# Kernel optimization log

Measured on AMD Instinct MI355X. Metric: run time of the kernel, lower is better.

## Reference

```python
import jax, jax.numpy as jnp
import numpy as np

NUM_NODES = 512
HEADS = 4
IN_F = 256
OUT_F = 128
EPS = 1e-5


def _layernorm(x, g, b):
    mu = jnp.mean(x, axis=-1, keepdims=True)
    var = jnp.mean(jnp.square(x - mu), axis=-1, keepdims=True)
    return (x - mu) * jax.lax.rsqrt(var + EPS) * g + b


def setup_inputs() -> dict:
    key = jax.random.key(0)
    ks = jax.random.split(key, 16)
    N = 32 * NUM_NODES
    E = 262144
    s = 0.05
    return {
        "x": jax.random.normal(ks[0], (N, IN_F), jnp.float32),
        "edge_index": jax.random.randint(ks[1], (2, E), 0, N, jnp.int64),
        "W_l": jax.random.normal(ks[2], (IN_F, HEADS * OUT_F), jnp.float32) * s,
        "W_r": jax.random.normal(ks[3], (IN_F, HEADS * OUT_F), jnp.float32) * s,
        "att": jax.random.normal(ks[4], (HEADS, OUT_F), jnp.float32) * s,
        "gat_bias": jnp.zeros((OUT_F,), jnp.float32),
        "gat_gamma": jnp.ones((OUT_F,), jnp.float32),
        "gat_beta": jnp.zeros((OUT_F,), jnp.float32),
        "cnn_W": jax.random.normal(ks[5], (IN_F, OUT_F), jnp.float32) * s,
        "cnn_b": jnp.zeros((OUT_F,), jnp.float32),
        "conv_W": jax.random.normal(ks[6], (OUT_F, OUT_F, 7), jnp.float32) * s,
        "conv_b": jnp.zeros((OUT_F,), jnp.float32),
        "cnn_gamma": jnp.ones((OUT_F,), jnp.float32),
        "cnn_beta": jnp.zeros((OUT_F,), jnp.float32),
        "res_W": jax.random.normal(ks[7], (IN_F, OUT_F), jnp.float32) * s,
        "res_b": jnp.zeros((OUT_F,), jnp.float32),
        "fuse_gamma": jnp.ones((OUT_F,), jnp.float32),
        "fuse_beta": jnp.zeros((OUT_F,), jnp.float32),
    }


def reference(x, edge_index, W_l, W_r, att, gat_bias, gat_gamma, gat_beta,
              cnn_W, cnn_b, conv_W, conv_b, cnn_gamma, cnn_beta,
              res_W, res_b, fuse_gamma, fuse_beta):
    N = x.shape[0]
    B = N // NUM_NODES
    # --- GATv2 branch (add self-loops like PyG default) ---
    loop = jnp.arange(N, dtype=edge_index.dtype)
    src = jnp.concatenate([edge_index[0], loop])
    dst = jnp.concatenate([edge_index[1], loop])
    x_l = (x @ W_l).reshape(N, HEADS, OUT_F)
    x_r = (x @ W_r).reshape(N, HEADS, OUT_F)
    e = x_l[src] + x_r[dst]                      # [E+N, H, F]
    e = jnp.where(e > 0, e, 0.2 * e)             # leaky_relu, slope 0.2
    score = jnp.einsum('ehf,hf->eh', e, att)     # [E+N, H]
    m = jax.ops.segment_max(score, dst, num_segments=N)
    ex = jnp.exp(score - m[dst])
    denom = jax.ops.segment_sum(ex, dst, num_segments=N)
    alpha = ex / denom[dst]
    agg = jax.ops.segment_sum(alpha[:, :, None] * x_l[src], dst, num_segments=N)
    h_gat = jnp.mean(agg, axis=1) + gat_bias     # concat=False -> head mean
    h_gat = jnp.where(h_gat > 0, h_gat, 0.01 * h_gat)  # nn.LeakyReLU default
    h_gat = _layernorm(h_gat, gat_gamma, gat_beta)
    # --- CNN branch ---
    xc = x @ cnn_W + cnn_b                       # [N, F]
    xc = xc.reshape(B, NUM_NODES, OUT_F).transpose(0, 2, 1)  # [B, F, L]
    hc = jax.lax.conv_general_dilated(xc, conv_W, window_strides=(1,),
                                      padding=[(3, 3)],
                                      dimension_numbers=('NCW', 'OIW', 'NCW'))
    hc = hc + conv_b[None, :, None]
    hc = hc.transpose(0, 2, 1).reshape(N, OUT_F)
    hc = jax.nn.relu(hc)
    hc = _layernorm(hc, cnn_gamma, cnn_beta)
    # --- fuse + residual ---
    h = h_gat + hc + (x @ res_W + res_b)
    return _layernorm(h, fuse_gamma, fuse_beta)
```

## Files before the change

### kernel.cpp

```cpp
#include <hip/hip_runtime.h>
#include <hip/hip_bf16.h>
#include <math.h>

#define IN_F 256
#define OUT_F 128
#define HEADS 4
#define HF 512
#define NCAT 1280

typedef __hip_bfloat16 bf16;
typedef unsigned short ushort_t;
typedef unsigned char uchar_t;

using bf16x8 = __attribute__((ext_vector_type(8))) short;
using f32x4  = __attribute__((ext_vector_type(4))) float;

__device__ __forceinline__ float bflo(unsigned u) { return __uint_as_float(u << 16); }
__device__ __forceinline__ float bfhi(unsigned u) { return __uint_as_float(u & 0xffff0000u); }
__device__ __forceinline__ float bf2f(ushort_t u) { return __uint_as_float((unsigned)u << 16); }
__device__ __forceinline__ ushort_t f2bf(float f) {
    __hip_bfloat16 h = __float2bfloat16(f);
    return *reinterpret_cast<ushort_t*>(&h);
}

__device__ __forceinline__ void gload16(const void* g, void* l) {
    __builtin_amdgcn_global_load_lds(
        (const __attribute__((address_space(1))) unsigned int*)g,
        (__attribute__((address_space(3))) unsigned int*)l, 16, 0, 0);
}

template <int CTRL>
__device__ __forceinline__ float dpp_add(float s) {
    int t = __builtin_amdgcn_update_dpp(0, __float_as_int(s), CTRL, 0xf, 0xf, true);
    return s + __int_as_float(t);
}
__device__ __forceinline__ float rowsum16(float s) {
    s = dpp_add<0x121>(s);
    s = dpp_add<0x122>(s);
    s = dpp_add<0x124>(s);
    s = dpp_add<0x128>(s);
    return s;
}

__global__ __launch_bounds__(256) void prep_kernel(
    const float* __restrict__ x, ushort_t* __restrict__ xb, int n_cvt,
    const float* __restrict__ Wl, const float* __restrict__ Wr,
    const float* __restrict__ Wc, const float* __restrict__ Wres,
    const float* __restrict__ Wconv,
    ushort_t* __restrict__ Wt, ushort_t* __restrict__ Wt2,
    const int* __restrict__ ei, int* __restrict__ counts, int E,
    int g1, int g2) {
    int b = blockIdx.x;
    if (b < g1) {
        int i = (b * 256 + threadIdx.x) * 8;
        if (i >= n_cvt) return;
        float4 a = *(const float4*)(x + i);
        float4 c = *(const float4*)(x + i + 4);
        uint4 o;
        o.x = f2bf(a.x) | ((unsigned)f2bf(a.y) << 16);
        o.y = f2bf(a.z) | ((unsigned)f2bf(a.w) << 16);
        o.z = f2bf(c.x) | ((unsigned)f2bf(c.y) << 16);
        o.w = f2bf(c.z) | ((unsigned)f2bf(c.w) << 16);
        *(uint4*)(xb + i) = o;
    } else if (b < g2) {
        int idx = (b - g1) * 256 + threadIdx.x;
        if (idx < NCAT * 256) {
            int n = idx >> 8, k = idx & 255;
            float v;
            if (n < 512)       v = Wl[(size_t)k * 512 + n];
            else if (n < 1024) v = Wr[(size_t)k * 512 + (n - 512)];
            else if (n < 1152) v = Wc[(size_t)k * 128 + (n - 1024)];
            else               v = Wres[(size_t)k * 128 + (n - 1152)];
            Wt[idx] = f2bf(v);
        } else {
            int j = idx - NCAT * 256;
            if (j < 7 * 128 * 128) {
                int k = j >> 14, o = (j >> 7) & 127, i = j & 127;
                Wt2[j] = f2bf(Wconv[((size_t)o * 128 + i) * 7 + k]);
            }
        }
    } else {
        int e = (b - g2) * 256 + threadIdx.x;
        if (e < E) atomicAdd(&counts[ei[E + e]], 1);
    }
}

__global__ __launch_bounds__(256) void gemm_scatter_kernel(
    const ushort_t* __restrict__ A,
    const ushort_t* __restrict__ Wt,
    uchar_t* __restrict__ xl8t, float* __restrict__ scales,
    ushort_t* __restrict__ xrb, ushort_t* __restrict__ xcb,
    ushort_t* __restrict__ resb,
    const int* __restrict__ ei, int* __restrict__ cursor,
    int* __restrict__ srcs, int E, int SB) {
    __shared__ __align__(1024) ushort_t As[128 * 64];
    __shared__ __align__(1024) ushort_t Bs[128 * 64];
    __shared__ float smax[128][2];
    if (blockIdx.x < SB) {
        int e = blockIdx.x * 256 + threadIdx.x;
        if (e < E) {
            int dd = ei[E + e];
            int pp = atomicAdd(&cursor[dd], 1);
            srcs[pp] = ei[e];
        }
        return;
    }
    int bid = blockIdx.x - SB;
    int by = bid / 10, bx = bid - by * 10;
    int tid = threadIdx.x;
    int lane = tid & 63, wid = tid >> 6;
    int wr = (wid >> 1) * 64, wc = (wid & 1) * 64;
    int brow = by * 128, bcol = bx * 128;
    int srow = lane >> 3;
    int sslot = lane & 7;
    int rl = lane & 15, kq = lane >> 4;
    f32x4 acc[4][4] = {};
    for (int k0 = 0; k0 < 256; k0 += 64) {
        #pragma unroll
        for (int j = 0; j < 4; ++j) {
            int r = (wid * 4 + j) * 8 + srow;
            int sl = sslot ^ (r & 7);
            gload16(A  + (size_t)(brow + r) * 256 + k0 + sl * 8,
                    (char*)As + (wid * 4 + j) * 1024);
            gload16(Wt + (size_t)(bcol + r) * 256 + k0 + sl * 8,
                    (char*)Bs + (wid * 4 + j) * 1024);
        }
        __syncthreads();
        #pragma unroll
        for (int ks = 0; ks < 2; ++ks) {
            int cb = ks * 64 + kq * 16;
            bf16x8 af[4], bfv[4];
            #pragma unroll
            for (int m = 0; m < 4; ++m) {
                int r = wr + m * 16 + rl;
                af[m] = *(const bf16x8*)((const char*)As + r * 128 + (cb ^ ((r & 7) << 4)));
            }
            #pragma unroll
            for (int n = 0; n < 4; ++n) {
                int r = wc + n * 16 + rl;
                bfv[n] = *(const bf16x8*)((const char*)Bs + r * 128 + (cb ^ ((r & 7) << 4)));
            }
            #pragma unroll
            for (int m = 0; m < 4; ++m)
                #pragma unroll
                for (int n = 0; n < 4; ++n)
                    acc[m][n] = __builtin_amdgcn_mfma_f32_16x16x32_bf16(
                        af[m], bfv[n], acc[m][n], 0, 0, 0);
        }
        __syncthreads();
    }
    int rowb = kq * 4;
    if (bcol < 512) {
        int head = bcol >> 7;
        float rmax[4][4];
        #pragma unroll
        for (int m = 0; m < 4; ++m)
            #pragma unroll
            for (int q = 0; q < 4; ++q) {
                float t = fabsf(acc[m][0][q]);
                t = fmaxf(t, fabsf(acc[m][1][q]));
                t = fmaxf(t, fabsf(acc[m][2][q]));
                t = fmaxf(t, fabsf(acc[m][3][q]));
                #pragma unroll
                for (int o = 1; o < 16; o <<= 1) t = fmaxf(t, __shfl_xor(t, o));
                rmax[m][q] = t;
            }
        if (rl == 0) {
            #pragma unroll
            for (int m = 0; m < 4; ++m)
                #pragma unroll
                for (int q = 0; q < 4; ++q)
                    smax[wr + m * 16 + rowb + q][wid & 1] = rmax[m][q];
        }
        __syncthreads();
        #pragma unroll
        for (int m = 0; m < 4; ++m)
            #pragma unroll
            for (int q = 0; q < 4; ++q) {
                int row = wr + m * 16 + rowb + q;
                float sm = fmaxf(fmaxf(smax[row][0], smax[row][1]), 1e-8f);
                float s = sm * (1.f / 127.f);
                float rs = 127.f / sm;
                if ((wid & 1) == 0 && rl == 0)
                    scales[(size_t)(brow + row) * 4 + head] = s;
                #pragma unroll
                for (int n = 0; n < 4; ++n) {
                    int col = bcol + wc + n * 16 + rl;
                    int qv = (int)rintf(acc[m][n][q] * rs) + 128;
                    xl8t[(size_t)(brow + row) * 512 + col] = (uchar_t)qv;
                }
            }
        return;
    }
    ushort_t* dstp; int cstride, cb2;
    if (bcol < 1024)      { dstp = xrb;  cstride = 512; cb2 = bcol - 512; }
    else if (bcol < 1152) { dstp = xcb;  cstride = 128; cb2 = bcol - 1024; }
    else                  { dstp = resb; cstride = 128; cb2 = bcol - 1152; }
    #pragma unroll
    for (int m = 0; m < 4; ++m)
        #pragma unroll
        for (int n = 0; n < 4; ++n) {
            int col = cb2 + wc + n * 16 + rl;
            #pragma unroll
            for (int q = 0; q < 4; ++q) {
                int row = brow + wr + m * 16 + rowb + q;
                dstp[(size_t)row * cstride + col] = f2bf(acc[m][n][q]);
            }
        }
}

__global__ __launch_bounds__(1024) void scan_kernel(
    const int* __restrict__ counts, int* __restrict__ offs,
    int* __restrict__ cursor, int N) {
    __shared__ int wsum[16];
    int t = threadIdx.x;
    int lane = t & 63, w = t >> 6;
    int base = t * 16;
    int local[16], s = 0;
    #pragma unroll
    for (int i = 0; i < 16; ++i) {
        int v = (base + i < N) ? counts[base + i] : 0;
        local[i] = v; s += v;
    }
    int sc = s;
    #pragma unroll
    for (int off = 1; off < 64; off <<= 1) {
        int v = __shfl_up(sc, off);
        if (lane >= off) sc += v;
    }
    if (lane == 63) wsum[w] = sc;
    __syncthreads();
    if (w == 0 && lane < 16) {
        int v = wsum[lane];
        int scv = v;
        #pragma unroll
        for (int off = 1; off < 16; off <<= 1) {
            int u = __shfl_up(scv, off);
            if (lane >= off) scv += u;
        }
        wsum[lane] = scv - v;
    }
    __syncthreads();
    int run = wsum[w] + sc - s;
    #pragma unroll
    for (int i = 0; i < 16; ++i) {
        if (base + i < N) { offs[base + i] = run; cursor[base + i] = run; }
        run += local[i];
    }
}

__global__ __launch_bounds__(256) void conv_ln_kernel(
    const ushort_t* __restrict__ xcb, const float* __restrict__ cnn_b,
    const ushort_t* __restrict__ Wt2, const float* __restrict__ conv_b,
    const float* __restrict__ cnn_gamma, const float* __restrict__ cnn_beta,
    ushort_t* __restrict__ hcn_ln) {
    __shared__ ushort_t As[38][136];
    __shared__ __align__(1024) ushort_t Bs[128 * 128];
    __shared__ float hbuf[32][129];
    int tid = threadIdx.x;
    int lane = tid & 63, wid = tid >> 6;
    int wr = (wid >> 1) * 16, wc = (wid & 1) * 64;
    int b = blockIdx.y, l0 = blockIdx.x * 32;
    for (int u = tid; u < 38 * 16; u += 256) {
        int r = u >> 4, seg = u & 15;
        int l = l0 - 3 + r;
        uint4 o4 = make_uint4(0, 0, 0, 0);
        if (l >= 0 && l < 512) {
            uint4 v = *(const uint4*)(xcb + (size_t)(b * 512 + l) * 128 + seg * 8);
            float4 b0 = *(const float4*)(cnn_b + seg * 8);
            float4 b1 = *(const float4*)(cnn_b + seg * 8 + 4);
            o4.x = f2bf(bflo(v.x) + b0.x) | ((unsigned)f2bf(bfhi(v.x) + b0.y) << 16);
            o4.y = f2bf(bflo(v.y) + b0.z) | ((unsigned)f2bf(bfhi(v.y) + b0.w) << 16);
            o4.z = f2bf(bflo(v.z) + b1.x) | ((unsigned)f2bf(bfhi(v.z) + b1.y) << 16);
            o4.w = f2bf(bflo(v.w) + b1.z) | ((unsigned)f2bf(bfhi(v.w) + b1.w) << 16);
        }
        *(uint4*)&As[r][seg * 8] = o4;
    }
    f32x4 acc[4] = {};
    int rl = lane & 15, kb = (lane >> 4) * 8;
    int sr4 = lane >> 4, ss = lane & 15;
    for (int k = 0; k < 7; ++k) {
        __syncthreads();
        #pragma unroll
        for (int j = 0; j < 8; ++j) {
            int r = (wid * 8 + j) * 4 + sr4;
            int sl = ss ^ (r & 15);
            gload16(Wt2 + ((size_t)(k * 128 + r)) * 128 + sl * 8,
                    (char*)Bs + (wid * 8 + j) * 1024);
        }
        __syncthreads();
        #pragma unroll
        for (int kk = 0; kk < 4; ++kk) {
            bf16x8 af = *(const bf16x8*)&As[wr + rl + k][kk * 32 + kb];
            int cbyte = kk * 64 + (lane >> 4) * 16;
            #pragma unroll
            for (int n = 0; n < 4; ++n) {
                int r = wc + n * 16 + rl;
                bf16x8 bfr = *(const bf16x8*)((const char*)Bs + r * 256
                                              + (cbyte ^ ((r & 15) << 4)));
                acc[n] = __builtin_amdgcn_mfma_f32_16x16x32_bf16(af, bfr, acc[n], 0, 0, 0);
            }
        }
    }
    __syncthreads();
    int rowb = (lane >> 4) * 4;
    #pragma unroll
    for (int n = 0; n < 4; ++n) {
        int col = wc + n * 16 + rl;
        float cb = conv_b[col];
        #pragma unroll
        for (int q = 0; q < 4; ++q) {
            int r = wr + rowb + q;
            hbuf[r][col] = fmaxf(acc[n][q] + cb, 0.f);
        }
    }
    __syncthreads();
    for (int r = wid * 8; r < wid * 8 + 8; ++r) {
        int grow = b * 512 + l0 + r;
        float h0 = hbuf[r][lane], h1 = hbuf[r][lane + 64];
        float s = h0 + h1;
        #pragma unroll
        for (int off = 32; off; off >>= 1) s += __shfl_xor(s, off);
        float mu = s * (1.f / 128.f);
        float d0 = h0 - mu, d1 = h1 - mu;
        float vs = d0 * d0 + d1 * d1;
        #pragma unroll
        for (int off = 32; off; off >>= 1) vs += __shfl_xor(vs, off);
        float inv = rsqrtf(vs * (1.f / 128.f) + 1e-5f);
        size_t base = (size_t)grow * 128;
        hcn_ln[base + lane]      = f2bf(d0 * inv * cnn_gamma[lane]      + cnn_beta[lane]);
        hcn_ln[base + lane + 64] = f2bf(d1 * inv * cnn_gamma[lane + 64] + cnn_beta[lane + 64]);
    }
}

__global__ __launch_bounds__(256) void gat_final_kernel(
    const uchar_t* __restrict__ xl8t, const float* __restrict__ scales,
    const ushort_t* __restrict__ xrb,
    const int* __restrict__ srcs, const int* __restrict__ offs,
    const float* __restrict__ att, const float* __restrict__ gat_bias,
    const float* __restrict__ gat_gamma, const float* __restrict__ gat_beta,
    const ushort_t* __restrict__ hcn_ln, const ushort_t* __restrict__ resb,
    const float* __restrict__ res_b,
    const float* __restrict__ fuse_gamma, const float* __restrict__ fuse_beta,
    float* __restrict__ out, int E, int N) {
    int wid = (blockIdx.x * 256 + threadIdx.x) >> 6;
    int lane = threadIdx.x & 63;
    if (wid >= N) return;
    int d = wid;
    int h = lane >> 4;
    const uint4 rv = ((const uint4*)(xrb + (size_t)d * HF))[lane];
    float xr8[8];
    xr8[0] = bflo(rv.x); xr8[1] = bfhi(rv.x);
    xr8[2] = bflo(rv.y); xr8[3] = bfhi(rv.y);
    xr8[4] = bflo(rv.z); xr8[5] = bfhi(rv.z);
    xr8[6] = bflo(rv.w); xr8[7] = bfhi(rv.w);
    const float LOG2E = 1.44269504f;
    const float4 a0 = ((const float4*)att)[lane * 2];
    const float4 a1 = ((const float4*)att)[lane * 2 + 1];
    const float aw[8] = {a0.x * LOG2E, a0.y * LOG2E, a0.z * LOG2E, a0.w * LOG2E,
                         a1.x * LOG2E, a1.y * LOG2E, a1.z * LOG2E, a1.w * LOG2E};
    float acc[8] = {};
    float dn = 0.f, sumexs = 0.f;

    auto process = [&](uint2 lv, float sc) {
        float qf[8];
        qf[0] = (float)(lv.x & 0xff);         qf[1] = (float)((lv.x >> 8) & 0xff);
        qf[2] = (float)((lv.x >> 16) & 0xff); qf[3] = (float)(lv.x >> 24);
        qf[4] = (float)(lv.y & 0xff);         qf[5] = (float)((lv.y >> 8) & 0xff);
        qf[6] = (float)((lv.y >> 16) & 0xff); qf[7] = (float)(lv.y >> 24);
        float c = 128.f * sc;
        float s1 = 0.f, s2 = 0.f;
        #pragma unroll
        for (int j = 0; j < 8; ++j) {
            float v = fmaf(sc, qf[j], xr8[j]) - c;
            s1 = fmaf(v, aw[j], s1);
            s2 = fmaf(fabsf(v), aw[j], s2);
        }
        float s = fmaf(0.6f, s1, 0.4f * s2);
        s = rowsum16(s);
        float ex = exp2f(s);
        float exs = ex * sc;
        dn += ex; sumexs += exs;
        #pragma unroll
        for (int j = 0; j < 8; ++j) acc[j] = fmaf(exs, qf[j], acc[j]);
    };

    process(((const uint2*)(xl8t + (size_t)d * 512))[lane],
            scales[(size_t)d * 4 + h]);

    int start = offs[d];
    int end = (d == N - 1) ? E : offs[d + 1];
    int nfull = (end - start) >> 2;
    int p = start;
    uint2 L0, L1, L2, L3;
    float C0, C1, C2, C3;
    if (nfull > 0) {
        int s0 = srcs[p], s1 = srcs[p + 1], s2 = srcs[p + 2], s3 = srcs[p + 3];
        L0 = ((const uint2*)(xl8t + (size_t)s0 * 512))[lane];
        L1 = ((const uint2*)(xl8t + (size_t)s1 * 512))[lane];
        L2 = ((const uint2*)(xl8t + (size_t)s2 * 512))[lane];
        L3 = ((const uint2*)(xl8t + (size_t)s3 * 512))[lane];
        C0 = scales[(size_t)s0 * 4 + h];
        C1 = scales[(size_t)s1 * 4 + h];
        C2 = scales[(size_t)s2 * 4 + h];
        C3 = scales[(size_t)s3 * 4 + h];
        p += 4;
    }
    for (int b = 1; b < nfull; ++b) {
        int s0 = srcs[p], s1 = srcs[p + 1], s2 = srcs[p + 2], s3 = srcs[p + 3];
        uint2 M0 = ((const uint2*)(xl8t + (size_t)s0 * 512))[lane];
        uint2 M1 = ((const uint2*)(xl8t + (size_t)s1 * 512))[lane];
        uint2 M2 = ((const uint2*)(xl8t + (size_t)s2 * 512))[lane];
        uint2 M3 = ((const uint2*)(xl8t + (size_t)s3 * 512))[lane];
        float D0 = scales[(size_t)s0 * 4 + h];
        float D1 = scales[(size_t)s1 * 4 + h];
        float D2 = scales[(size_t)s2 * 4 + h];
        float D3 = scales[(size_t)s3 * 4 + h];
        p += 4;
        process(L0, C0); process(L1, C1); process(L2, C2); process(L3, C3);
        L0 = M0; L1 = M1; L2 = M2; L3 = M3;
        C0 = D0; C1 = D1; C2 = D2; C3 = D3;
    }
    if (nfull > 0) {
        process(L0, C0); process(L1, C1); process(L2, C2); process(L3, C3);
    }
    for (; p < end; ++p) {
        int sp = srcs[p];
        process(((const uint2*)(xl8t + (size_t)sp * 512))[lane],
                scales[(size_t)sp * 4 + h]);
    }

    float inv = 1.f / dn;
    float corr = 128.f * sumexs;
    float v[8];
    #pragma unroll
    for (int j = 0; j < 8; ++j) {
        float t2 = (acc[j] - corr) * inv;
        t2 += __shfl_xor(t2, 16);
        t2 += __shfl_xor(t2, 32);
        v[j] = t2;
    }
    int col = (lane & 15) * 8 + 2 * h;
    float g0 = 0.25f * v[2 * h]     + gat_bias[col];
    float g1 = 0.25f * v[2 * h + 1] + gat_bias[col + 1];
    g0 = g0 > 0.f ? g0 : 0.01f * g0;
    g1 = g1 > 0.f ? g1 : 0.01f * g1;
    float s = g0 + g1;
    #pragma unroll
    for (int off = 32; off; off >>= 1) s += __shfl_xor(s, off);
    float mu = s * (1.f / 128.f);
    float d0 = g0 - mu, d1 = g1 - mu;
    float vs = d0 * d0 + d1 * d1;
    #pragma unroll
    for (int off = 32; off; off >>= 1) vs += __shfl_xor(vs, off);
    float rinv = rsqrtf(vs * (1.f / 128.f) + 1e-5f);
    float hg0 = d0 * rinv * gat_gamma[col]     + gat_beta[col];
    float hg1 = d1 * rinv * gat_gamma[col + 1] + gat_beta[col + 1];
    size_t base = (size_t)d * 128 + col;
    unsigned hcu = *(const unsigned*)(hcn_ln + base);
    unsigned rsu = *(const unsigned*)(resb + base);
    float v0 = hg0 + bflo(hcu) + bflo(rsu) + res_b[col];
    float v1 = hg1 + bfhi(hcu) + bfhi(rsu) + res_b[col + 1];
    s = v0 + v1;
    #pragma unroll
    for (int off = 32; off; off >>= 1) s += __shfl_xor(s, off);
    mu = s * (1.f / 128.f);
    d0 = v0 - mu; d1 = v1 - mu;
    vs = d0 * d0 + d1 * d1;
    #pragma unroll
    for (int off = 32; off; off >>= 1) vs += __shfl_xor(vs, off);
    rinv = rsqrtf(vs * (1.f / 128.f) + 1e-5f);
    float2 o2 = make_float2(d0 * rinv * fuse_gamma[col]     + fuse_beta[col],
                            d1 * rinv * fuse_gamma[col + 1] + fuse_beta[col + 1]);
    *(float2*)(out + base) = o2;
}

extern "C" void kernel_launch(void* const* d_in, const int* in_sizes, int n_in,
                              void* d_out, int out_size, void* d_ws, size_t ws_size,
                              hipStream_t stream) {
    const float* x         = (const float*)d_in[0];
    const int*   ei        = (const int*)d_in[1];
    const float* W_l       = (const float*)d_in[2];
    const float* W_r       = (const float*)d_in[3];
    const float* att       = (const float*)d_in[4];
    const float* gat_bias  = (const float*)d_in[5];
    const float* gat_gamma = (const float*)d_in[6];
    const float* gat_beta  = (const float*)d_in[7];
    const float* cnn_W     = (const float*)d_in[8];
    const float* cnn_b     = (const float*)d_in[9];
    const float* conv_W    = (const float*)d_in[10];
    const float* conv_b    = (const float*)d_in[11];
    const float* cnn_gamma = (const float*)d_in[12];
    const float* cnn_beta  = (const float*)d_in[13];
    const float* res_W     = (const float*)d_in[14];
    const float* res_b     = (const float*)d_in[15];
    const float* fuse_gamma= (const float*)d_in[16];
    const float* fuse_beta = (const float*)d_in[17];

    int N = in_sizes[0] / IN_F;
    int E = in_sizes[1] / 2;

    char* ws = (char*)d_ws;
    size_t off = 0;
    ushort_t* xb     = (ushort_t*)(ws + off); off += (size_t)N * IN_F * 2;
    ushort_t* Wt     = (ushort_t*)(ws + off); off += (size_t)NCAT * IN_F * 2;
    ushort_t* Wt2    = (ushort_t*)(ws + off); off += (size_t)7 * 128 * 128 * 2;
    uchar_t*  xl8t   = (uchar_t*)(ws + off);  off += (size_t)N * HF;
    float*    scales = (float*)(ws + off);    off += (size_t)N * 4 * 4;
    ushort_t* xrb    = (ushort_t*)(ws + off); off += (size_t)N * HF * 2;
    ushort_t* xcb    = (ushort_t*)(ws + off); off += (size_t)N * 128 * 2;
    ushort_t* resb   = (ushort_t*)(ws + off); off += (size_t)N * 128 * 2;
    ushort_t* hcn_ln = (ushort_t*)(ws + off); off += (size_t)N * 128 * 2;
    int*  counts     = (int*)(ws + off);  off += (size_t)N * 4;
    int*  offs       = (int*)(ws + off);  off += (size_t)N * 4;
    int*  cursor     = (int*)(ws + off);  off += (size_t)N * 4;
    int*  srcs       = (int*)(ws + off);  off += (size_t)E * 4;

    hipMemsetAsync(counts, 0, (size_t)N * 4, stream);

    dim3 blk(256);
    int n_cvt = N * IN_F;
    int g1 = (n_cvt / 8 + 255) / 256;
    int g2 = g1 + (NCAT * 256 + 7 * 128 * 128 + 255) / 256;
    int g3 = g2 + (E + 255) / 256;
    prep_kernel<<<g3, blk, 0, stream>>>(x, xb, n_cvt,
        W_l, W_r, cnn_W, res_W, conv_W, Wt, Wt2, ei, counts, E, g1, g2);

    scan_kernel<<<1, 1024, 0, stream>>>(counts, offs, cursor, N);

    int SB = (E + 255) / 256;
    gemm_scatter_kernel<<<SB + (NCAT / 128) * (N / 128), blk, 0, stream>>>(
        xb, Wt, xl8t, scales, xrb, xcb, resb, ei, cursor, srcs, E, SB);

    conv_ln_kernel<<<dim3(16, 32), blk, 0, stream>>>(
        xcb, cnn_b, Wt2, conv_b, cnn_gamma, cnn_beta, hcn_ln);

    gat_final_kernel<<<(N + 3) / 4, blk, 0, stream>>>(
        xl8t, scales, xrb, srcs, offs, att, gat_bias, gat_gamma, gat_beta,
        hcn_ln, resb, res_b, fuse_gamma, fuse_beta, (float*)d_out, E, N);
}
```

Baseline: 139.5 us.

## Precompute per-source attention dot in GEMM epilogue and move fuse LayerNorm into conv kernel

The leaky-relu score is split as 0.6*(a·x) + 0.4*|x|·a. The source half a·x_l is computed once per node and head in the GEMM epilogue and stored next to the int8 scale as a float2. This removes one FMA chain per element per edge in the GAT inner loop, at the cost of an extra 8-byte load per edge. The final residual+LayerNorm fusion also moves from the GAT kernel into the conv kernel, so the kernel order becomes GAT then conv_fuse, with an intermediate bf16 GAT output buffer replacing the CNN one.

```diff
diff --git a/kernel.cpp b/kernel.cpp
--- a/kernel.cpp
+++ b/kernel.cpp
@@ -88,7 +88,8 @@
 __global__ __launch_bounds__(256) void gemm_scatter_kernel(
     const ushort_t* __restrict__ A,
     const ushort_t* __restrict__ Wt,
-    uchar_t* __restrict__ xl8t, float* __restrict__ scales,
+    const float* __restrict__ att,
+    uchar_t* __restrict__ xl8t, float2* __restrict__ saxl,
     ushort_t* __restrict__ xrb, ushort_t* __restrict__ xcb,
     ushort_t* __restrict__ resb,
     const int* __restrict__ ei, int* __restrict__ cursor,
@@ -96,6 +97,7 @@
     __shared__ __align__(1024) ushort_t As[128 * 64];
     __shared__ __align__(1024) ushort_t Bs[128 * 64];
     __shared__ float smax[128][2];
+    __shared__ float paxl[128][2];
     if (blockIdx.x < SB) {
         int e = blockIdx.x * 256 + threadIdx.x;
         if (e < E) {
@@ -152,7 +154,9 @@
     int rowb = kq * 4;
     if (bcol < 512) {
         int head = bcol >> 7;
-        float rmax[4][4];
+        float at[4];
+        #pragma unroll
+        for (int n = 0; n < 4; ++n) at[n] = att[bcol + wc + n * 16 + rl];
         #pragma unroll
         for (int m = 0; m < 4; ++m)
             #pragma unroll
@@ -163,15 +167,17 @@
                 t = fmaxf(t, fabsf(acc[m][3][q]));
                 #pragma unroll
                 for (int o = 1; o < 16; o <<= 1) t = fmaxf(t, __shfl_xor(t, o));
-                rmax[m][q] = t;
-            }
-        if (rl == 0) {
-            #pragma unroll
-            for (int m = 0; m < 4; ++m)
+                float p = 0.f;
                 #pragma unroll
-                for (int q = 0; q < 4; ++q)
-                    smax[wr + m * 16 + rowb + q][wid & 1] = rmax[m][q];
-        }
+                for (int n = 0; n < 4; ++n) p = fmaf(at[n], acc[m][n][q], p);
+                #pragma unroll
+                for (int o = 1; o < 16; o <<= 1) p += __shfl_xor(p, o);
+                if (rl == 0) {
+                    int row = wr + m * 16 + rowb + q;
+                    smax[row][wid & 1] = t;
+                    paxl[row][wid & 1] = p;
+                }
+            }
         __syncthreads();
         #pragma unroll
         for (int m = 0; m < 4; ++m)
@@ -181,8 +187,10 @@
                 float sm = fmaxf(fmaxf(smax[row][0], smax[row][1]), 1e-8f);
                 float s = sm * (1.f / 127.f);
                 float rs = 127.f / sm;
-                if ((wid & 1) == 0 && rl == 0)
-                    scales[(size_t)(brow + row) * 4 + head] = s;
+                if ((wid & 1) == 0 && rl == 0) {
+                    float axlf = 0.6f * 1.44269504f * (paxl[row][0] + paxl[row][1]);
+                    saxl[(size_t)(brow + row) * 4 + head] = make_float2(s, axlf);
+                }
                 #pragma unroll
                 for (int n = 0; n < 4; ++n) {
                     int col = bcol + wc + n * 16 + rl;
@@ -249,11 +257,153 @@
     }
 }
 
-__global__ __launch_bounds__(256) void conv_ln_kernel(
+__global__ __launch_bounds__(256) void gat_kernel(
+    const uchar_t* __restrict__ xl8t, const float2* __restrict__ saxl,
+    const ushort_t* __restrict__ xrb,
+    const int* __restrict__ srcs, const int* __restrict__ offs,
+    const float* __restrict__ att, const float* __restrict__ gat_bias,
+    const float* __restrict__ gat_gamma, const float* __restrict__ gat_beta,
+    ushort_t* __restrict__ hgat_ln, int E, int N) {
+    int wid = (blockIdx.x * 256 + threadIdx.x) >> 6;
+    int lane = threadIdx.x & 63;
+    if (wid >= N) return;
+    int d = wid;
+    int h = lane >> 4;
+    const uint4 rv = ((const uint4*)(xrb + (size_t)d * HF))[lane];
+    float xr8[8];
+    xr8[0] = bflo(rv.x); xr8[1] = bfhi(rv.x);
+    xr8[2] = bflo(rv.y); xr8[3] = bfhi(rv.y);
+    xr8[4] = bflo(rv.z); xr8[5] = bfhi(rv.z);
+    xr8[6] = bflo(rv.w); xr8[7] = bfhi(rv.w);
+    const float LOG2E = 1.44269504f;
+    const float4 a0 = ((const float4*)att)[lane * 2];
+    const float4 a1 = ((const float4*)att)[lane * 2 + 1];
+    const float aw[8] = {a0.x * LOG2E, a0.y * LOG2E, a0.z * LOG2E, a0.w * LOG2E,
+                         a1.x * LOG2E, a1.y * LOG2E, a1.z * LOG2E, a1.w * LOG2E};
+    float awm[8];
+    #pragma unroll
+    for (int j = 0; j < 8; ++j) awm[j] = 0.4f * aw[j];
+    float axr_l = 0.f;
+    #pragma unroll
+    for (int j = 0; j < 8; ++j) axr_l = fmaf(aw[j], xr8[j], axr_l);
+    float axrf = 0.6f * rowsum16(axr_l);
+
+    float acc[8] = {};
+    float dn = 0.f, sumexs = 0.f;
+
+    auto process = [&](uint2 lv, float sc, float axlf) {
+        float qf[8];
+        qf[0] = (float)(lv.x & 0xff);         qf[1] = (float)((lv.x >> 8) & 0xff);
+        qf[2] = (float)((lv.x >> 16) & 0xff); qf[3] = (float)(lv.x >> 24);
+        qf[4] = (float)(lv.y & 0xff);         qf[5] = (float)((lv.y >> 8) & 0xff);
+        qf[6] = (float)((lv.y >> 16) & 0xff); qf[7] = (float)(lv.y >> 24);
+        float c = 128.f * sc;
+        float s2a = 0.f, s2b = 0.f;
+        #pragma unroll
+        for (int j = 0; j < 4; ++j) {
+            float v = fmaf(sc, qf[j], xr8[j]) - c;
+            s2a = fmaf(fabsf(v), awm[j], s2a);
+        }
+        #pragma unroll
+        for (int j = 4; j < 8; ++j) {
+            float v = fmaf(sc, qf[j], xr8[j]) - c;
+            s2b = fmaf(fabsf(v), awm[j], s2b);
+        }
+        float s = axlf + axrf + rowsum16(s2a + s2b);
+        float ex = exp2f(s);
+        float exs = ex * sc;
+        dn += ex; sumexs += exs;
+        #pragma unroll
+        for (int j = 0; j < 8; ++j) acc[j] = fmaf(exs, qf[j], acc[j]);
+    };
+
+    {
+        float2 sa = saxl[(size_t)d * 4 + h];
+        process(((const uint2*)(xl8t + (size_t)d * 512))[lane], sa.x, sa.y);
+    }
+
+    int start = offs[d];
+    int end = (d == N - 1) ? E : offs[d + 1];
+    int nfull = (end - start) >> 2;
+    int p = start;
+    uint2 L0, L1, L2, L3;
+    float2 S0, S1, S2, S3;
+    if (nfull > 0) {
+        int s0 = srcs[p], s1 = srcs[p + 1], s2 = srcs[p + 2], s3 = srcs[p + 3];
+        L0 = ((const uint2*)(xl8t + (size_t)s0 * 512))[lane];
+        L1 = ((const uint2*)(xl8t + (size_t)s1 * 512))[lane];
+        L2 = ((const uint2*)(xl8t + (size_t)s2 * 512))[lane];
+        L3 = ((const uint2*)(xl8t + (size_t)s3 * 512))[lane];
+        S0 = saxl[(size_t)s0 * 4 + h];
+        S1 = saxl[(size_t)s1 * 4 + h];
+        S2 = saxl[(size_t)s2 * 4 + h];
+        S3 = saxl[(size_t)s3 * 4 + h];
+        p += 4;
+    }
+    for (int b = 1; b < nfull; ++b) {
+        int s0 = srcs[p], s1 = srcs[p + 1], s2 = srcs[p + 2], s3 = srcs[p + 3];
+        uint2 M0 = ((const uint2*)(xl8t + (size_t)s0 * 512))[lane];
+        uint2 M1 = ((const uint2*)(xl8t + (size_t)s1 * 512))[lane];
+        uint2 M2 = ((const uint2*)(xl8t + (size_t)s2 * 512))[lane];
+        uint2 M3 = ((const uint2*)(xl8t + (size_t)s3 * 512))[lane];
+        float2 T0 = saxl[(size_t)s0 * 4 + h];
+        float2 T1 = saxl[(size_t)s1 * 4 + h];
+        float2 T2 = saxl[(size_t)s2 * 4 + h];
+        float2 T3 = saxl[(size_t)s3 * 4 + h];
+        p += 4;
+        process(L0, S0.x, S0.y); process(L1, S1.x, S1.y);
+        process(L2, S2.x, S2.y); process(L3, S3.x, S3.y);
+        L0 = M0; L1 = M1; L2 = M2; L3 = M3;
+        S0 = T0; S1 = T1; S2 = T2; S3 = T3;
+    }
+    if (nfull > 0) {
+        process(L0, S0.x, S0.y); process(L1, S1.x, S1.y);
+        process(L2, S2.x, S2.y); process(L3, S3.x, S3.y);
+    }
+    for (; p < end; ++p) {
+        int sp = srcs[p];
+        float2 sa = saxl[(size_t)sp * 4 + h];
+        process(((const uint2*)(xl8t + (size_t)sp * 512))[lane], sa.x, sa.y);
+    }
+
+    float inv = 1.f / dn;
+    float corr = 128.f * sumexs;
+    float v[8];
+    #pragma unroll
+    for (int j = 0; j < 8; ++j) {
+        float t2 = (acc[j] - corr) * inv;
+        t2 += __shfl_xor(t2, 16);
+        t2 += __shfl_xor(t2, 32);
+        v[j] = t2;
+    }
+    int col = (lane & 15) * 8 + 2 * h;
+    float g0 = 0.25f * v[2 * h]     + gat_bias[col];
+    float g1 = 0.25f * v[2 * h + 1] + gat_bias[col + 1];
+    g0 = g0 > 0.f ? g0 : 0.01f * g0;
+    g1 = g1 > 0.f ? g1 : 0.01f * g1;
+    float s = g0 + g1;
+    #pragma unroll
+    for (int off = 32; off; off >>= 1) s += __shfl_xor(s, off);
+    float mu = s * (1.f / 128.f);
+    float d0 = g0 - mu, d1 = g1 - mu;
+    float vs = d0 * d0 + d1 * d1;
+    #pragma unroll
+    for (int off = 32; off; off >>= 1) vs += __shfl_xor(vs, off);
+    float rinv = rsqrtf(vs * (1.f / 128.f) + 1e-5f);
+    float o0 = d0 * rinv * gat_gamma[col]     + gat_beta[col];
+    float o1 = d1 * rinv * gat_gamma[col + 1] + gat_beta[col + 1];
+    unsigned pk = (unsigned)f2bf(o0) | ((unsigned)f2bf(o1) << 16);
+    *(unsigned*)(hgat_ln + (size_t)d * 128 + col) = pk;
+}
+
+__global__ __launch_bounds__(256) void conv_fuse_kernel(
     const ushort_t* __restrict__ xcb, const float* __restrict__ cnn_b,
     const ushort_t* __restrict__ Wt2, const float* __restrict__ conv_b,
     const float* __restrict__ cnn_gamma, const float* __restrict__ cnn_beta,
-    ushort_t* __restrict__ hcn_ln) {
+    const ushort_t* __restrict__ hgat_ln, const ushort_t* __restrict__ resb,
+    const float* __restrict__ res_b,
+    const float* __restrict__ fuse_gamma, const float* __restrict__ fuse_beta,
+    float* __restrict__ out) {
     __shared__ ushort_t As[38][136];
     __shared__ __align__(1024) ushort_t Bs[128 * 128];
     __shared__ float hbuf[32][129];
@@ -327,152 +477,25 @@
         #pragma unroll
         for (int off = 32; off; off >>= 1) vs += __shfl_xor(vs, off);
         float inv = rsqrtf(vs * (1.f / 128.f) + 1e-5f);
+        float hcn0 = d0 * inv * cnn_gamma[lane]      + cnn_beta[lane];
+        float hcn1 = d1 * inv * cnn_gamma[lane + 64] + cnn_beta[lane + 64];
         size_t base = (size_t)grow * 128;
-        hcn_ln[base + lane]      = f2bf(d0 * inv * cnn_gamma[lane]      + cnn_beta[lane]);
-        hcn_ln[base + lane + 64] = f2bf(d1 * inv * cnn_gamma[lane + 64] + cnn_beta[lane + 64]);
-    }
-}
-
-__global__ __launch_bounds__(256) void gat_final_kernel(
-    const uchar_t* __restrict__ xl8t, const float* __restrict__ scales,
-    const ushort_t* __restrict__ xrb,
-    const int* __restrict__ srcs, const int* __restrict__ offs,
-    const float* __restrict__ att, const float* __restrict__ gat_bias,
-    const float* __restrict__ gat_gamma, const float* __restrict__ gat_beta,
-    const ushort_t* __restrict__ hcn_ln, const ushort_t* __restrict__ resb,
-    const float* __restrict__ res_b,
-    const float* __restrict__ fuse_gamma, const float* __restrict__ fuse_beta,
-    float* __restrict__ out, int E, int N) {
-    int wid = (blockIdx.x * 256 + threadIdx.x) >> 6;
-    int lane = threadIdx.x & 63;
-    if (wid >= N) return;
-    int d = wid;
-    int h = lane >> 4;
-    const uint4 rv = ((const uint4*)(xrb + (size_t)d * HF))[lane];
-    float xr8[8];
-    xr8[0] = bflo(rv.x); xr8[1] = bfhi(rv.x);
-    xr8[2] = bflo(rv.y); xr8[3] = bfhi(rv.y);
-    xr8[4] = bflo(rv.z); xr8[5] = bfhi(rv.z);
-    xr8[6] = bflo(rv.w); xr8[7] = bfhi(rv.w);
-    const float LOG2E = 1.44269504f;
-    const float4 a0 = ((const float4*)att)[lane * 2];
-    const float4 a1 = ((const float4*)att)[lane * 2 + 1];
-    const float aw[8] = {a0.x * LOG2E, a0.y * LOG2E, a0.z * LOG2E, a0.w * LOG2E,
-                         a1.x * LOG2E, a1.y * LOG2E, a1.z * LOG2E, a1.w * LOG2E};
-    float acc[8] = {};
-    float dn = 0.f, sumexs = 0.f;
-
-    auto process = [&](uint2 lv, float sc) {
-        float qf[8];
-        qf[0] = (float)(lv.x & 0xff);         qf[1] = (float)((lv.x >> 8) & 0xff);
-        qf[2] = (float)((lv.x >> 16) & 0xff); qf[3] = (float)(lv.x >> 24);
-        qf[4] = (float)(lv.y & 0xff);         qf[5] = (float)((lv.y >> 8) & 0xff);
-        qf[6] = (float)((lv.y >> 16) & 0xff); qf[7] = (float)(lv.y >> 24);
-        float c = 128.f * sc;
-        float s1 = 0.f, s2 = 0.f;
-        #pragma unroll
-        for (int j = 0; j < 8; ++j) {
-            float v = fmaf(sc, qf[j], xr8[j]) - c;
-            s1 = fmaf(v, aw[j], s1);
-            s2 = fmaf(fabsf(v), aw[j], s2);
-        }
-        float s = fmaf(0.6f, s1, 0.4f * s2);
-        s = rowsum16(s);
-        float ex = exp2f(s);
-        float exs = ex * sc;
-        dn += ex; sumexs += exs;
-        #pragma unroll
-        for (int j = 0; j < 8; ++j) acc[j] = fmaf(exs, qf[j], acc[j]);
-    };
-
-    process(((const uint2*)(xl8t + (size_t)d * 512))[lane],
-            scales[(size_t)d * 4 + h]);
-
-    int start = offs[d];
-    int end = (d == N - 1) ? E : offs[d + 1];
-    int nfull = (end - start) >> 2;
-    int p = start;
-    uint2 L0, L1, L2, L3;
-    float C0, C1, C2, C3;
-    if (nfull > 0) {
-        int s0 = srcs[p], s1 = srcs[p + 1], s2 = srcs[p + 2], s3 = srcs[p + 3];
-        L0 = ((const uint2*)(xl8t + (size_t)s0 * 512))[lane];
-        L1 = ((const uint2*)(xl8t + (size_t)s1 * 512))[lane];
-        L2 = ((const uint2*)(xl8t + (size_t)s2 * 512))[lane];
-        L3 = ((const uint2*)(xl8t + (size_t)s3 * 512))[lane];
-        C0 = scales[(size_t)s0 * 4 + h];
-        C1 = scales[(size_t)s1 * 4 + h];
-        C2 = scales[(size_t)s2 * 4 + h];
-        C3 = scales[(size_t)s3 * 4 + h];
-        p += 4;
-    }
-    for (int b = 1; b < nfull; ++b) {
-        int s0 = srcs[p], s1 = srcs[p + 1], s2 = srcs[p + 2], s3 = srcs[p + 3];
-        uint2 M0 = ((const uint2*)(xl8t + (size_t)s0 * 512))[lane];
-        uint2 M1 = ((const uint2*)(xl8t + (size_t)s1 * 512))[lane];
-        uint2 M2 = ((const uint2*)(xl8t + (size_t)s2 * 512))[lane];
-        uint2 M3 = ((const uint2*)(xl8t + (size_t)s3 * 512))[lane];
-        float D0 = scales[(size_t)s0 * 4 + h];
-        float D1 = scales[(size_t)s1 * 4 + h];
-        float D2 = scales[(size_t)s2 * 4 + h];
-        float D3 = scales[(size_t)s3 * 4 + h];
-        p += 4;
-        process(L0, C0); process(L1, C1); process(L2, C2); process(L3, C3);
-        L0 = M0; L1 = M1; L2 = M2; L3 = M3;
-        C0 = D0; C1 = D1; C2 = D2; C3 = D3;
-    }
-    if (nfull > 0) {
-        process(L0, C0); process(L1, C1); process(L2, C2); process(L3, C3);
-    }
-    for (; p < end; ++p) {
-        int sp = srcs[p];
-        process(((const uint2*)(xl8t + (size_t)sp * 512))[lane],
-                scales[(size_t)sp * 4 + h]);
-    }
-
-    float inv = 1.f / dn;
-    float corr = 128.f * sumexs;
-    float v[8];
-    #pragma unroll
-    for (int j = 0; j < 8; ++j) {
-        float t2 = (acc[j] - corr) * inv;
-        t2 += __shfl_xor(t2, 16);
-        t2 += __shfl_xor(t2, 32);
-        v[j] = t2;
-    }
-    int col = (lane & 15) * 8 + 2 * h;
-    float g0 = 0.25f * v[2 * h]     + gat_bias[col];
-    float g1 = 0.25f * v[2 * h + 1] + gat_bias[col + 1];
-    g0 = g0 > 0.f ? g0 : 0.01f * g0;
-    g1 = g1 > 0.f ? g1 : 0.01f * g1;
-    float s = g0 + g1;
-    #pragma unroll
-    for (int off = 32; off; off >>= 1) s += __shfl_xor(s, off);
-    float mu = s * (1.f / 128.f);
-    float d0 = g0 - mu, d1 = g1 - mu;
-    float vs = d0 * d0 + d1 * d1;
-    #pragma unroll
-    for (int off = 32; off; off >>= 1) vs += __shfl_xor(vs, off);
-    float rinv = rsqrtf(vs * (1.f / 128.f) + 1e-5f);
-    float hg0 = d0 * rinv * gat_gamma[col]     + gat_beta[col];
-    float hg1 = d1 * rinv * gat_gamma[col + 1] + gat_beta[col + 1];
-    size_t base = (size_t)d * 128 + col;
-    unsigned hcu = *(const unsigned*)(hcn_ln + base);
-    unsigned rsu = *(const unsigned*)(resb + base);
-    float v0 = hg0 + bflo(hcu) + bflo(rsu) + res_b[col];
-    float v1 = hg1 + bfhi(hcu) + bfhi(rsu) + res_b[col + 1];
-    s = v0 + v1;
-    #pragma unroll
-    for (int off = 32; off; off >>= 1) s += __shfl_xor(s, off);
-    mu = s * (1.f / 128.f);
-    d0 = v0 - mu; d1 = v1 - mu;
-    vs = d0 * d0 + d1 * d1;
-    #pragma unroll
-    for (int off = 32; off; off >>= 1) vs += __shfl_xor(vs, off);
-    rinv = rsqrtf(vs * (1.f / 128.f) + 1e-5f);
-    float2 o2 = make_float2(d0 * rinv * fuse_gamma[col]     + fuse_beta[col],
-                            d1 * rinv * fuse_gamma[col + 1] + fuse_beta[col + 1]);
-    *(float2*)(out + base) = o2;
+        float v0 = bf2f(hgat_ln[base + lane])      + hcn0
+                 + bf2f(resb[base + lane])      + res_b[lane];
+        float v1 = bf2f(hgat_ln[base + lane + 64]) + hcn1
+                 + bf2f(resb[base + lane + 64]) + res_b[lane + 64];
+        s = v0 + v1;
+        #pragma unroll
+        for (int off = 32; off; off >>= 1) s += __shfl_xor(s, off);
+        mu = s * (1.f / 128.f);
+        d0 = v0 - mu; d1 = v1 - mu;
+        vs = d0 * d0 + d1 * d1;
+        #pragma unroll
+        for (int off = 32; off; off >>= 1) vs += __shfl_xor(vs, off);
+        inv = rsqrtf(vs * (1.f / 128.f) + 1e-5f);
+        out[base + lane]      = d0 * inv * fuse_gamma[lane]      + fuse_beta[lane];
+        out[base + lane + 64] = d1 * inv * fuse_gamma[lane + 64] + fuse_beta[lane + 64];
+    }
 }
 
 extern "C" void kernel_launch(void* const* d_in, const int* in_sizes, int n_in,
@@ -506,11 +529,11 @@
     ushort_t* Wt     = (ushort_t*)(ws + off); off += (size_t)NCAT * IN_F * 2;
     ushort_t* Wt2    = (ushort_t*)(ws + off); off += (size_t)7 * 128 * 128 * 2;
     uchar_t*  xl8t   = (uchar_t*)(ws + off);  off += (size_t)N * HF;
-    float*    scales = (float*)(ws + off);    off += (size_t)N * 4 * 4;
+    float2*   saxl   = (float2*)(ws + off);   off += (size_t)N * 4 * 8;
     ushort_t* xrb    = (ushort_t*)(ws + off); off += (size_t)N * HF * 2;
     ushort_t* xcb    = (ushort_t*)(ws + off); off += (size_t)N * 128 * 2;
     ushort_t* resb   = (ushort_t*)(ws + off); off += (size_t)N * 128 * 2;
-    ushort_t* hcn_ln = (ushort_t*)(ws + off); off += (size_t)N * 128 * 2;
+    ushort_t* hgat_ln= (ushort_t*)(ws + off); off += (size_t)N * 128 * 2;
     int*  counts     = (int*)(ws + off);  off += (size_t)N * 4;
     int*  offs       = (int*)(ws + off);  off += (size_t)N * 4;
     int*  cursor     = (int*)(ws + off);  off += (size_t)N * 4;
@@ -530,12 +553,13 @@
 
     int SB = (E + 255) / 256;
     gemm_scatter_kernel<<<SB + (NCAT / 128) * (N / 128), blk, 0, stream>>>(
-        xb, Wt, xl8t, scales, xrb, xcb, resb, ei, cursor, srcs, E, SB);
-
-    conv_ln_kernel<<<dim3(16, 32), blk, 0, stream>>>(
-        xcb, cnn_b, Wt2, conv_b, cnn_gamma, cnn_beta, hcn_ln);
-
-    gat_final_kernel<<<(N + 3) / 4, blk, 0, stream>>>(
-        xl8t, scales, xrb, srcs, offs, att, gat_bias, gat_gamma, gat_beta,
-        hcn_ln, resb, res_b, fuse_gamma, fuse_beta, (float*)d_out, E, N);
-}
+        xb, Wt, att, xl8t, saxl, xrb, xcb, resb, ei, cursor, srcs, E, SB);
+
+    gat_kernel<<<(N + 3) / 4, blk, 0, stream>>>(
+        xl8t, saxl, xrb, srcs, offs, att, gat_bias, gat_gamma, gat_beta,
+        hgat_ln, E, N);
+
+    conv_fuse_kernel<<<dim3(16, 32), blk, 0, stream>>>(
+        xcb, cnn_b, Wt2, conv_b, cnn_gamma, cnn_beta,
+        hgat_ln, resb, res_b, fuse_gamma, fuse_beta, (float*)d_out);
+}
```

New measurement: 153.5 us. +10.1%, slower.
